# Optimization experiments

Hardware: AMD Instinct MI355X
Metric: run time of the kernel (lower is better)

The kernel has to match this reference:

```python
import jax, jax.numpy as jnp
import numpy as np

WIDTH = 8    # hwcfg['width']: bitstream code width, BinGen scale = 2**WIDTH
DEPTH = 12   # hwcfg['depth']: FSUAdd accumulator depth, bound = 2**DEPTH - 1


def setup_inputs() -> dict:
    key = jax.random.key(0)
    k1, k2 = jax.random.split(key)
    batch, in_f, out_f = 4096, 2048, 4096
    # stochastic-computing input: one bit per element for the current cycle
    x = jax.random.bernoulli(k1, 0.5, (batch, in_f)).astype(jnp.float32)
    # bipolar weight probabilities in [-1, 1] (weight_ext)
    w = jax.random.uniform(k2, (out_f, in_f), jnp.float32, -1.0, 1.0)
    # Sobol RNG sample for the current cycle, values live in [0, 2**WIDTH)
    rng_val = jnp.ones((1,), jnp.float32) * 128.0
    return {"input": x, "weight": w, "rng_val": rng_val}


def reference(input, weight, rng_val):
    """One cycle of FSUMatMul: static bipolar FSUMul + scaled bipolar FSUAdd (first cycle, acc=0)."""
    batch, in_f = input.shape
    # ---- FSUMul (static, bipolar) ----
    prob = (weight + 1.0) * 0.5                      # bipolar value -> unipolar probability
    source = jnp.round(prob * (2.0 ** WIDTH))        # BinGen: quantized binary source
    path = (source > rng_val[0]).astype(input.dtype)  # BSGen bit for each weight, (out, in)
    # product bit = XNOR(x, path) = 1 - |x - path| on {0,1} bits.
    # Sum over in_features of the (batch,out,in) broadcast product, computed exactly
    # via the GEMM identity: sum_k 1-|x-p| = in_f - (sum x + sum p - 2 * x @ p^T).
    sx = jnp.sum(input, axis=1)                      # (batch,)
    sp = jnp.sum(path, axis=1)                       # (out,)
    xp = jnp.einsum('bi,oi->bo', input, path)        # (batch, out) GEMM
    sum_prod = in_f - (sx[:, None] + sp[None, :] - 2.0 * xp)
    # ---- FSUAdd (bipolar, scaled: scale_carry = entry = in_f -> offset = 0) ----
    scale_carry = jnp.float32(in_f)
    acc = jnp.clip(sum_prod, 0.0, 2.0 ** DEPTH - 1)  # first-cycle accumulator state (init 0)
    out = (acc >= scale_carry).astype(jnp.float32)   # emitted output bit per (batch, out)
    return out
```

## Files before the change

### kernel.cpp

```cpp
#include <hip/hip_runtime.h>


#define BATCH 4096
#define INF   2048
#define OUTF  4096
#define WORDS 32
#define NX_CHUNKS ((BATCH * INF) / 256)
#define NW_CHUNKS ((OUTF  * INF) / 256)

__global__ __launch_bounds__(256) void pack_kernel(
    const float* __restrict__ x, const float* __restrict__ w,
    const float* __restrict__ rng,
    unsigned long long* __restrict__ xp, unsigned long long* __restrict__ pp)
{
    const int tid  = threadIdx.x;
    const int wav  = tid >> 6;
    const int lane = tid & 63;
    const int chunk = blockIdx.x * 4 + wav;
    const float r = rng[0];

    if (chunk < NX_CHUNKS) {
        const float4 v = *reinterpret_cast<const float4*>(
            x + (size_t)chunk * 256 + lane * 4);
        unsigned long long b0 = __ballot(v.x != 0.0f);
        unsigned long long b1 = __ballot(v.y != 0.0f);
        unsigned long long b2 = __ballot(v.z != 0.0f);
        unsigned long long b3 = __ballot(v.w != 0.0f);
        if (lane == 0) {
            size_t base = (size_t)chunk * 4;
            xp[base + 0] = b0; xp[base + 1] = b1;
            xp[base + 2] = b2; xp[base + 3] = b3;
        }
    } else {
        const int c2 = chunk - NX_CHUNKS;
        const float4 v = *reinterpret_cast<const float4*>(
            w + (size_t)c2 * 256 + lane * 4);
        float s0 = rintf((v.x + 1.0f) * 0.5f * 256.0f);
        float s1 = rintf((v.y + 1.0f) * 0.5f * 256.0f);
        float s2 = rintf((v.z + 1.0f) * 0.5f * 256.0f);
        float s3 = rintf((v.w + 1.0f) * 0.5f * 256.0f);
        unsigned long long b0 = __ballot(s0 > r);
        unsigned long long b1 = __ballot(s1 > r);
        unsigned long long b2 = __ballot(s2 > r);
        unsigned long long b3 = __ballot(s3 > r);
        const int o  = c2 >> 3;
        const int rr = c2 & 7;
        if (lane == 0) {
            pp[(size_t)(rr * 4 + 0) * OUTF + o] = b0;
            pp[(size_t)(rr * 4 + 1) * OUTF + o] = b1;
            pp[(size_t)(rr * 4 + 2) * OUTF + o] = b2;
            pp[(size_t)(rr * 4 + 3) * OUTF + o] = b3;
        }
    }
}

__global__ __launch_bounds__(256) void cmp_kernel(
    const unsigned long long* __restrict__ xp,
    const unsigned long long* __restrict__ pp,
    float* __restrict__ out)
{
    const int tid = threadIdx.x;
    const int o0  = (blockIdx.x * 256 + tid) * 4;
    const int b0  = blockIdx.y * 16;

    const unsigned long long p0 = pp[o0 + 0];
    const unsigned long long p1 = pp[o0 + 1];
    const unsigned long long p2 = pp[o0 + 2];
    const unsigned long long p3 = pp[o0 + 3];

    for (int i = 0; i < 16; ++i) {
        const int b = b0 + i;
        const unsigned long long xw = xp[(size_t)b * WORDS];
        bool e0 = (p0 == xw);
        bool e1 = (p1 == xw);
        bool e2 = (p2 == xw);
        bool e3 = (p3 == xw);
        if (__any(e0 | e1 | e2 | e3)) {
            for (int wd = 1; wd < WORDS; ++wd) {
                const unsigned long long xx = xp[(size_t)b * WORDS + wd];
                const unsigned long long* prow = pp + (size_t)wd * OUTF + o0;
                e0 = e0 && (prow[0] == xx);
                e1 = e1 && (prow[1] == xx);
                e2 = e2 && (prow[2] == xx);
                e3 = e3 && (prow[3] == xx);
            }
        }
        float4 res = make_float4(e0 ? 1.0f : 0.0f, e1 ? 1.0f : 0.0f,
                                 e2 ? 1.0f : 0.0f, e3 ? 1.0f : 0.0f);
        *reinterpret_cast<float4*>(out + (size_t)b * OUTF + o0) = res;
    }
}

extern "C" void kernel_launch(void* const* d_in, const int* in_sizes, int n_in,
                              void* d_out, int out_size, void* d_ws, size_t ws_size,
                              hipStream_t stream) {
    const float* x   = (const float*)d_in[0];
    const float* w   = (const float*)d_in[1];
    const float* rng = (const float*)d_in[2];
    float* out = (float*)d_out;

    unsigned long long* xp = (unsigned long long*)d_ws;
    unsigned long long* pp = xp + (size_t)BATCH * WORDS;

    pack_kernel<<<dim3((NX_CHUNKS + NW_CHUNKS) / 4), dim3(256), 0, stream>>>(
        x, w, rng, xp, pp);

    cmp_kernel<<<dim3(OUTF / 1024, BATCH / 16), dim3(256), 0, stream>>>(
        xp, pp, out);
}
```

Baseline: 131.2 us.

## Pack only first 64 bits per row and verify rare matches from raw inputs

The pack kernel now builds a single 64-bit signature per input row and per weight row from the first 64 columns, instead of packing all 2048 columns. The compare kernel uses that signature as a filter. Only when a signature matches does it re-check the remaining columns straight from the float inputs, recomputing the weight bits on the fly. The aim is to avoid reading and packing the full x and w matrices, cutting most of the input traffic. The cost is an uncoalesced, divergent slow path that would get expensive if many prefixes matched.

```diff
diff --git a/kernel.cpp b/kernel.cpp
--- a/kernel.cpp
+++ b/kernel.cpp
@@ -4,89 +4,70 @@
 #define BATCH 4096
 #define INF   2048
 #define OUTF  4096
-#define WORDS 32
-#define NX_CHUNKS ((BATCH * INF) / 256)
-#define NW_CHUNKS ((OUTF  * INF) / 256)
 
-__global__ __launch_bounds__(256) void pack_kernel(
+__global__ __launch_bounds__(256) void pack0_kernel(
     const float* __restrict__ x, const float* __restrict__ w,
     const float* __restrict__ rng,
-    unsigned long long* __restrict__ xp, unsigned long long* __restrict__ pp)
+    unsigned long long* __restrict__ xp0, unsigned long long* __restrict__ pp0)
 {
-    const int tid  = threadIdx.x;
-    const int wav  = tid >> 6;
-    const int lane = tid & 63;
-    const int chunk = blockIdx.x * 4 + wav;
-    const float r = rng[0];
+    const int lane = threadIdx.x & 63;
+    const int wav  = threadIdx.x >> 6;
+    const int id   = blockIdx.x * 4 + wav;
 
-    if (chunk < NX_CHUNKS) {
-        const float4 v = *reinterpret_cast<const float4*>(
-            x + (size_t)chunk * 256 + lane * 4);
-        unsigned long long b0 = __ballot(v.x != 0.0f);
-        unsigned long long b1 = __ballot(v.y != 0.0f);
-        unsigned long long b2 = __ballot(v.z != 0.0f);
-        unsigned long long b3 = __ballot(v.w != 0.0f);
-        if (lane == 0) {
-            size_t base = (size_t)chunk * 4;
-            xp[base + 0] = b0; xp[base + 1] = b1;
-            xp[base + 2] = b2; xp[base + 3] = b3;
-        }
+    if (id < BATCH) {
+        const float v = x[(size_t)id * INF + lane];
+        const unsigned long long b = __ballot(v != 0.0f);
+        if (lane == 0) xp0[id] = b;
     } else {
-        const int c2 = chunk - NX_CHUNKS;
-        const float4 v = *reinterpret_cast<const float4*>(
-            w + (size_t)c2 * 256 + lane * 4);
-        float s0 = rintf((v.x + 1.0f) * 0.5f * 256.0f);
-        float s1 = rintf((v.y + 1.0f) * 0.5f * 256.0f);
-        float s2 = rintf((v.z + 1.0f) * 0.5f * 256.0f);
-        float s3 = rintf((v.w + 1.0f) * 0.5f * 256.0f);
-        unsigned long long b0 = __ballot(s0 > r);
-        unsigned long long b1 = __ballot(s1 > r);
-        unsigned long long b2 = __ballot(s2 > r);
-        unsigned long long b3 = __ballot(s3 > r);
-        const int o  = c2 >> 3;
-        const int rr = c2 & 7;
-        if (lane == 0) {
-            pp[(size_t)(rr * 4 + 0) * OUTF + o] = b0;
-            pp[(size_t)(rr * 4 + 1) * OUTF + o] = b1;
-            pp[(size_t)(rr * 4 + 2) * OUTF + o] = b2;
-            pp[(size_t)(rr * 4 + 3) * OUTF + o] = b3;
-        }
+        const int o = id - BATCH;
+        const float v = w[(size_t)o * INF + lane];
+        const float s = rintf((v + 1.0f) * 0.5f * 256.0f);
+        const unsigned long long b = __ballot(s > rng[0]);
+        if (lane == 0) pp0[o] = b;
     }
 }
 
 __global__ __launch_bounds__(256) void cmp_kernel(
-    const unsigned long long* __restrict__ xp,
-    const unsigned long long* __restrict__ pp,
+    const unsigned long long* __restrict__ xp0,
+    const unsigned long long* __restrict__ pp0,
+    const float* __restrict__ x, const float* __restrict__ w,
+    const float* __restrict__ rng,
     float* __restrict__ out)
 {
     const int tid = threadIdx.x;
     const int o0  = (blockIdx.x * 256 + tid) * 4;
     const int b0  = blockIdx.y * 16;
 
-    const unsigned long long p0 = pp[o0 + 0];
-    const unsigned long long p1 = pp[o0 + 1];
-    const unsigned long long p2 = pp[o0 + 2];
-    const unsigned long long p3 = pp[o0 + 3];
+    const unsigned long long p0 = pp0[o0 + 0];
+    const unsigned long long p1 = pp0[o0 + 1];
+    const unsigned long long p2 = pp0[o0 + 2];
+    const unsigned long long p3 = pp0[o0 + 3];
 
     for (int i = 0; i < 16; ++i) {
         const int b = b0 + i;
-        const unsigned long long xw = xp[(size_t)b * WORDS];
-        bool e0 = (p0 == xw);
-        bool e1 = (p1 == xw);
-        bool e2 = (p2 == xw);
-        bool e3 = (p3 == xw);
-        if (__any(e0 | e1 | e2 | e3)) {
-            for (int wd = 1; wd < WORDS; ++wd) {
-                const unsigned long long xx = xp[(size_t)b * WORDS + wd];
-                const unsigned long long* prow = pp + (size_t)wd * OUTF + o0;
-                e0 = e0 && (prow[0] == xx);
-                e1 = e1 && (prow[1] == xx);
-                e2 = e2 && (prow[2] == xx);
-                e3 = e3 && (prow[3] == xx);
+        const unsigned long long xw = xp0[b];
+        bool eq[4];
+        eq[0] = (p0 == xw);
+        eq[1] = (p1 == xw);
+        eq[2] = (p2 == xw);
+        eq[3] = (p3 == xw);
+        if (eq[0] | eq[1] | eq[2] | eq[3]) {
+            const float r = rng[0];
+            for (int j = 0; j < 4; ++j) {
+                if (!eq[j]) continue;
+                const int o = o0 + j;
+                bool all = true;
+                for (int k = 64; k < INF; ++k) {
+                    const bool xb = x[(size_t)b * INF + k] != 0.0f;
+                    const bool pb =
+                        rintf((w[(size_t)o * INF + k] + 1.0f) * 0.5f * 256.0f) > r;
+                    all = all && (xb == pb);
+                }
+                eq[j] = all;
             }
         }
-        float4 res = make_float4(e0 ? 1.0f : 0.0f, e1 ? 1.0f : 0.0f,
-                                 e2 ? 1.0f : 0.0f, e3 ? 1.0f : 0.0f);
+        float4 res = make_float4(eq[0] ? 1.0f : 0.0f, eq[1] ? 1.0f : 0.0f,
+                                 eq[2] ? 1.0f : 0.0f, eq[3] ? 1.0f : 0.0f);
         *reinterpret_cast<float4*>(out + (size_t)b * OUTF + o0) = res;
     }
 }
@@ -99,12 +80,12 @@
     const float* rng = (const float*)d_in[2];
     float* out = (float*)d_out;
 
-    unsigned long long* xp = (unsigned long long*)d_ws;
-    unsigned long long* pp = xp + (size_t)BATCH * WORDS;
+    unsigned long long* xp0 = (unsigned long long*)d_ws;
+    unsigned long long* pp0 = xp0 + BATCH;
 
-    pack_kernel<<<dim3((NX_CHUNKS + NW_CHUNKS) / 4), dim3(256), 0, stream>>>(
-        x, w, rng, xp, pp);
+    pack0_kernel<<<dim3((BATCH + OUTF) / 4), dim3(256), 0, stream>>>(
+        x, w, rng, xp0, pp0);
 
     cmp_kernel<<<dim3(OUTF / 1024, BATCH / 16), dim3(256), 0, stream>>>(
-        xp, pp, out);
+        xp0, pp0, x, w, rng, out);
 }
```

Result: faster. 108.1 us (-17.6%).
